# Kernel tuning notes

Hardware: AMD Instinct MI355X
Metric: run time of the kernel (lower is better)

## Reference

```python
import jax, jax.numpy as jnp
import numpy as np

N_NODES = 50000
N_EDGES = 800000
MUL = 32            # multiplicity of 0e and 1o feature irreps
N_SPECIES = 4       # node_attr = 4x0e one-hot
N_BASIS = 8         # radial basis scalars
N_HID = 8           # invariant_neurons
AVG_NEIGH = 16.0
INV_SQRT3 = 1.0 / np.sqrt(3.0).astype(np.float32)


def setup_inputs() -> dict:
    key = jax.random.key(0)
    ks = jax.random.split(key, 16)
    x = jax.random.normal(ks[0], (N_NODES, MUL * 4), jnp.float32)  # 32x0e + 32x1o
    species = jax.random.randint(ks[1], (N_NODES,), 0, N_SPECIES)
    node_attr = jax.nn.one_hot(species, N_SPECIES, dtype=jnp.float32)
    edge_embedding = jax.random.normal(ks[2], (N_EDGES, N_BASIS), jnp.float32)
    edge_attr = jax.random.normal(ks[3], (N_EDGES, 4), jnp.float32)  # 1x0e + 1x1o
    edge_index = jax.random.randint(ks[4], (2, N_EDGES), 0, N_NODES)
    # learned params
    W_lin1_s = jax.random.normal(ks[5], (MUL, MUL), jnp.float32)
    W_lin1_v = jax.random.normal(ks[6], (MUL, MUL), jnp.float32)
    fc_w1 = jax.random.normal(ks[7], (N_BASIS, N_HID), jnp.float32)
    fc_w2 = jax.random.normal(ks[8], (N_HID, 4 * MUL), jnp.float32)  # tp.weight_numel = 4*MUL
    W_lin2_s = jax.random.normal(ks[9], (2 * MUL, MUL), jnp.float32)  # mid simplify: 64x0e
    W_lin2_v = jax.random.normal(ks[10], (2 * MUL, MUL), jnp.float32)  # 64x1o
    W_sc_s = jax.random.normal(ks[11], (MUL, N_SPECIES, MUL), jnp.float32)
    W_sc_v = jax.random.normal(ks[12], (MUL, N_SPECIES, MUL), jnp.float32)
    return dict(node_features=x, node_attr=node_attr, edge_embedding=edge_embedding,
                edge_attr=edge_attr, edge_index=edge_index,
                W_lin1_s=W_lin1_s, W_lin1_v=W_lin1_v, fc_w1=fc_w1, fc_w2=fc_w2,
                W_lin2_s=W_lin2_s, W_lin2_v=W_lin2_v, W_sc_s=W_sc_s, W_sc_v=W_sc_v)


def _forward(node_features, node_attr, edge_embedding, edge_attr, edge_index,
             W_lin1_s, W_lin1_v, fc_w1, fc_w2, W_lin2_s, W_lin2_v, W_sc_s, W_sc_v):
    n = node_features.shape[0]
    xs = node_features[:, :MUL]                       # [N, 32] scalars (0e)
    xv = node_features[:, MUL:].reshape(n, MUL, 3)    # [N, 32, 3] vectors (1o)

    # self-connection: FullyConnectedTensorProduct(feat, 4x0e -> feat), uvw weights
    sc_norm = 1.0 / np.sqrt(MUL * N_SPECIES).astype(np.float32)
    sc_s = jnp.einsum('nu,nv,uvw->nw', xs, node_attr, W_sc_s) * sc_norm
    sc_v = jnp.einsum('nui,nv,uvw->nwi', xv, node_attr, W_sc_v) * sc_norm

    # linear_1: per-irrep channel mixing, 1/sqrt(fan_in)
    l1n = 1.0 / np.sqrt(MUL).astype(np.float32)
    ys = (xs @ W_lin1_s) * l1n
    yv = jnp.einsum('nui,uw->nwi', xv, W_lin1_v) * l1n

    # radial MLP -> per-edge tensor-product weights (4 paths x MUL)
    h = jax.nn.silu((edge_embedding @ fc_w1) / np.sqrt(N_BASIS).astype(np.float32))
    w = (h @ fc_w2) / np.sqrt(N_HID).astype(np.float32)  # [E, 128]
    w00, w01, w10, w11 = jnp.split(w, 4, axis=1)          # instruction order (0,0),(0,1),(1,0),(1,1)

    src = edge_index[0]
    dst = edge_index[1]
    es = ys[src]                                          # [E, 32]
    ev = yv[src]                                          # [E, 32, 3]
    a0 = edge_attr[:, 0]                                  # [E]    0e
    a1 = edge_attr[:, 1:4]                                # [E, 3] 1o

    # per-edge weighted uvu tensor product paths
    o_s_a = w00 * es * a0[:, None]                                       # 0e x 0e -> 0e
    o_s_b = w11 * jnp.einsum('eui,ei->eu', ev, a1) * INV_SQRT3           # 1o x 1o -> 0e
    o_v_a = (w01 * es)[:, :, None] * a1[:, None, :]                      # 0e x 1o -> 1o
    o_v_b = w10[:, :, None] * ev * a0[:, None, None]                     # 1o x 0e -> 1o

    # scatter-sum to destination nodes
    mid_s = jax.ops.segment_sum(jnp.concatenate([o_s_a, o_s_b], axis=1), dst, num_segments=n)
    mid_v = jax.ops.segment_sum(jnp.concatenate([o_v_a, o_v_b], axis=1), dst, num_segments=n)
    inv = 1.0 / np.sqrt(AVG_NEIGH).astype(np.float32)
    mid_s = mid_s * inv   # [N, 64]
    mid_v = mid_v * inv   # [N, 64, 3]

    # linear_2: 64x0e+64x1o -> 32x0e+32x1o
    l2n = 1.0 / np.sqrt(2 * MUL).astype(np.float32)
    out_s = (mid_s @ W_lin2_s) * l2n + sc_s
    out_v = jnp.einsum('nui,uw->nwi', mid_v, W_lin2_v) * l2n + sc_v
    return jnp.concatenate([out_s, out_v.reshape(n, MUL * 3)], axis=1)


def reference(node_features, node_attr, edge_embedding, edge_attr, edge_index,
              W_lin1_s, W_lin1_v, fc_w1, fc_w2, W_lin2_s, W_lin2_v, W_sc_s, W_sc_v):
    return _forward(node_features, node_attr, edge_embedding, edge_attr, edge_index,
                    W_lin1_s, W_lin1_v, fc_w1, fc_w2, W_lin2_s, W_lin2_v, W_sc_s, W_sc_v)
```

## Files before the change

### kernel.cpp

```cpp
#include <hip/hip_runtime.h>
#include <hip/hip_bf16.h>

#define N_NODES 50000
#define N_EDGES 800000
#define CAP 64
#define NODE_BLOCKS 1250
#define BUCKET_BLOCKS (N_EDGES/256)

__device__ __forceinline__ unsigned short f2bf(float f) {
    union { float f; unsigned u; } t; t.f = f;
    unsigned r = t.u + 0x7FFF + ((t.u >> 16) & 1);
    return (unsigned short)(r >> 16);
}

__global__ __launch_bounds__(256) void bucket_kernel(
    const int* __restrict__ eidx,
    int* __restrict__ counts, int* __restrict__ bucket)
{
    const int e = blockIdx.x * 256 + threadIdx.x;
    const int dst = eidx[N_EDGES + e];
    const int slot = atomicAdd(&counts[dst], 1);
    if (slot < CAP) bucket[(long)dst * CAP + slot] = e;
}

__global__ __launch_bounds__(256) void node_kernel(
    const float* __restrict__ x, const float* __restrict__ attr,
    const float* __restrict__ W1s, const float* __restrict__ W1v,
    const float* __restrict__ Wscs, const float* __restrict__ Wscv,
    unsigned short* __restrict__ ysvh, float* __restrict__ out)
{
    __shared__ float shm[10240];
    const int tid = threadIdx.x;
    const int nl = tid >> 5;
    const int w  = tid & 31;

    float w1s[32], w1v[32];
    #pragma unroll
    for (int u = 0; u < 32; ++u) {
        w1s[u] = W1s[u*32 + w];
        w1v[u] = W1v[u*32 + w];
    }
    #pragma unroll
    for (int i = 0; i < 4; ++i) {
        ((float4*)(shm + 2048))[tid + i*256] = ((const float4*)Wscs)[tid + i*256];
        ((float4*)(shm + 6144))[tid + i*256] = ((const float4*)Wscv)[tid + i*256];
    }

    const float l1n = 0.17677669529663687f;
    const float scn = 0.08838834764831843f;

    for (int batch = 0; batch < 5; ++batch) {
        const int node0 = blockIdx.x * 40 + batch * 8;
        float* xbuf = shm + (batch & 1) * 1024;
        ((float4*)xbuf)[tid] = ((const float4*)(x + (long)node0 * 128))[tid];
        __syncthreads();

        const int node = node0 + nl;
        const float* at = attr + (long)node * 4;
        int sp = 0;
        if (at[1] > 0.5f) sp = 1;
        if (at[2] > 0.5f) sp = 2;
        if (at[3] > 0.5f) sp = 3;

        const float* lx   = xbuf + nl * 128;
        const float* lscs = shm + 2048 + sp * 32;
        const float* lscv = shm + 6144 + sp * 32;

        float ys = 0.f, yv0 = 0.f, yv1 = 0.f, yv2 = 0.f;
        float ss = 0.f, sv0 = 0.f, sv1 = 0.f, sv2 = 0.f;
        #pragma unroll
        for (int u4 = 0; u4 < 8; ++u4) {
            const float4 xs4 = ((const float4*)lx)[u4];
            const float4 q0  = ((const float4*)(lx + 32))[u4*3 + 0];
            const float4 q1  = ((const float4*)(lx + 32))[u4*3 + 1];
            const float4 q2  = ((const float4*)(lx + 32))[u4*3 + 2];
            const float xsv[4]  = {xs4.x, xs4.y, xs4.z, xs4.w};
            const float xvv[12] = {q0.x,q0.y,q0.z,q0.w,
                                   q1.x,q1.y,q1.z,q1.w,
                                   q2.x,q2.y,q2.z,q2.w};
            #pragma unroll
            for (int j = 0; j < 4; ++j) {
                const int u = u4*4 + j;
                const float wss = lscs[u*128 + w];
                const float wsv = lscv[u*128 + w];
                ys  += xsv[j] * w1s[u];
                yv0 += xvv[3*j+0] * w1v[u];
                yv1 += xvv[3*j+1] * w1v[u];
                yv2 += xvv[3*j+2] * w1v[u];
                ss  += xsv[j] * wss;
                sv0 += xvv[3*j+0] * wsv;
                sv1 += xvv[3*j+1] * wsv;
                sv2 += xvv[3*j+2] * wsv;
            }
        }

        uint2 pk;
        pk.x = (unsigned)f2bf(ys  * l1n) | ((unsigned)f2bf(yv0 * l1n) << 16);
        pk.y = (unsigned)f2bf(yv1 * l1n) | ((unsigned)f2bf(yv2 * l1n) << 16);
        *(uint2*)(ysvh + (long)node * 128 + w * 4) = pk;

        float* op = out + (long)node * 128;
        op[w] = ss * scn;
        op[32 + 3*w + 0] = sv0 * scn;
        op[32 + 3*w + 1] = sv1 * scn;
        op[32 + 3*w + 2] = sv2 * scn;
    }
}

__global__ __launch_bounds__(256) void agg_kernel(
    const float* __restrict__ ee, const float* __restrict__ eattr,
    const int* __restrict__ eidx,
    const float* __restrict__ fcw1, const float* __restrict__ fcw2,
    const float* __restrict__ W2s, const float* __restrict__ W2v,
    const unsigned short* __restrict__ ysvh,
    const int* __restrict__ counts, const int* __restrict__ bucket,
    float* __restrict__ out)
{
    __shared__ float hrec[8][32 * 12];
    __shared__ float mid[8][256];

    const int tid = threadIdx.x;
    const int nl = tid >> 5;
    const int u  = tid & 31;
    const int node = blockIdx.x * 8 + nl;
    const float inv_sqrt8 = 0.35355339059327373f;

    float f2r[8][4];
    #pragma unroll
    for (int j = 0; j < 8; ++j) {
        f2r[j][0] = fcw2[j*128 + u];
        f2r[j][1] = fcw2[j*128 + 32 + u];
        f2r[j][2] = fcw2[j*128 + 64 + u];
        f2r[j][3] = fcw2[j*128 + 96 + u];
    }

    const int cnt = min(counts[node], CAP);
    int e0 = bucket[(long)node * CAP + u];
    const bool dummy = (u >= cnt);
    if (dummy) e0 = 0;
    int s0 = eidx[e0];

    {
        const float4 ea = ((const float4*)(ee + (long)e0 * 8))[0];
        const float4 eb = ((const float4*)(ee + (long)e0 * 8))[1];
        const float4 at = ((const float4*)eattr)[e0];
        const float eev[8] = {ea.x, ea.y, ea.z, ea.w, eb.x, eb.y, eb.z, eb.w};
        float* hr = hrec[nl] + u * 12;
        float h[8];
        #pragma unroll
        for (int j = 0; j < 8; ++j) {
            float pre = 0.f;
            #pragma unroll
            for (int b = 0; b < 8; ++b) pre += eev[b] * fcw1[b*8 + j];
            pre *= inv_sqrt8;
            const float s = pre / (1.f + __expf(-pre)) * inv_sqrt8;
            h[j] = dummy ? 0.f : s;
        }
        ((float4*)hr)[0] = make_float4(h[0], h[1], h[2], h[3]);
        ((float4*)hr)[1] = make_float4(h[4], h[5], h[6], h[7]);
        ((float4*)hr)[2] = at;
    }

    float msa = 0.f, msb = 0.f;
    float va0 = 0.f, va1 = 0.f, va2 = 0.f;
    float vb0 = 0.f, vb1 = 0.f, vb2 = 0.f;

    #define ACCUM(HA, HB, AT, Y)                                             \
    {                                                                        \
        const float es = __uint_as_float((Y).x << 16);                       \
        const float ex = __uint_as_float((Y).x & 0xffff0000u);               \
        const float ey = __uint_as_float((Y).y << 16);                       \
        const float ez = __uint_as_float((Y).y & 0xffff0000u);               \
        const float hh[8] = {HA.x,HA.y,HA.z,HA.w,HB.x,HB.y,HB.z,HB.w};       \
        float w00=0.f, w01=0.f, w10=0.f, w11=0.f;                            \
        _Pragma("unroll")                                                    \
        for (int j = 0; j < 8; ++j) {                                        \
            w00 += hh[j]*f2r[j][0]; w01 += hh[j]*f2r[j][1];                  \
            w10 += hh[j]*f2r[j][2]; w11 += hh[j]*f2r[j][3];                  \
        }                                                                    \
        const float a0 = AT.x, a1x = AT.y, a1y = AT.z, a1z = AT.w;           \
        msa += w00 * es * a0;                                                \
        msb += w11 * (ex*a1x + ey*a1y + ez*a1z);                             \
        const float t = w01 * es;                                            \
        va0 += t*a1x; va1 += t*a1y; va2 += t*a1z;                            \
        const float s = w10 * a0;                                            \
        vb0 += s*ex; vb1 += s*ey; vb2 += s*ez;                               \
    }

    #define GATHER(SLOT) \
        (*(const uint2*)(ysvh + (long)__shfl(s0, (SLOT), 32) * 128 + u * 4))

    const int c0 = min(cnt, 32);
    {
        uint2 y0 = GATHER(0), y1 = GATHER(1), y2 = GATHER(2), y3 = GATHER(3);
        for (int k = 0; k < c0; k += 4) {
            const int kn = (k + 4) & 31;
            const uint2 n0 = GATHER(kn);
            const uint2 n1 = GATHER(kn + 1);
            const uint2 n2 = GATHER(kn + 2);
            const uint2 n3 = GATHER(kn + 3);
            const float4* h0p = (const float4*)(hrec[nl] + (k + 0) * 12);
            const float4* h1p = (const float4*)(hrec[nl] + (k + 1) * 12);
            const float4* h2p = (const float4*)(hrec[nl] + (k + 2) * 12);
            const float4* h3p = (const float4*)(hrec[nl] + (k + 3) * 12);
            const float4 A0 = h0p[0], B0 = h0p[1], T0 = h0p[2];
            const float4 A1 = h1p[0], B1 = h1p[1], T1 = h1p[2];
            const float4 A2 = h2p[0], B2 = h2p[1], T2 = h2p[2];
            const float4 A3 = h3p[0], B3 = h3p[1], T3 = h3p[2];
            ACCUM(A0, B0, T0, y0)
            ACCUM(A1, B1, T1, y1)
            ACCUM(A2, B2, T2, y2)
            ACCUM(A3, B3, T3, y3)
            y0 = n0; y1 = n1; y2 = n2; y3 = n3;
        }
    }

    if (cnt > 32) {
        int be = bucket[(long)node * CAP + 32 + u];
        if (32 + u >= cnt) be = 0;
        for (int k = 32; k < cnt; ++k) {
            const int e = __shfl(be, k - 32, 32);
            const int s = eidx[e];
            const float4 ea = ((const float4*)(ee + (long)e * 8))[0];
            const float4 eb = ((const float4*)(ee + (long)e * 8))[1];
            const float4 at = ((const float4*)eattr)[e];
            const float eev[8] = {ea.x, ea.y, ea.z, ea.w, eb.x, eb.y, eb.z, eb.w};
            float h[8];
            #pragma unroll
            for (int j = 0; j < 8; ++j) {
                float pre = 0.f;
                #pragma unroll
                for (int b = 0; b < 8; ++b) pre += eev[b] * fcw1[b*8 + j];
                pre *= inv_sqrt8;
                h[j] = pre / (1.f + __expf(-pre)) * inv_sqrt8;
            }
            const float4 HA = make_float4(h[0], h[1], h[2], h[3]);
            const float4 HB = make_float4(h[4], h[5], h[6], h[7]);
            const uint2 y = *(const uint2*)(ysvh + (long)s * 128 + u * 4);
            ACCUM(HA, HB, at, y)
        }
    }
    #undef GATHER
    #undef ACCUM

    msb *= 0.5773502691896258f;

    float* m = mid[nl];
    m[u]       = msa;
    m[32 + u]  = msb;
    m[64  + u*3 + 0] = va0;  m[64  + u*3 + 1] = va1;  m[64  + u*3 + 2] = va2;
    m[160 + u*3 + 0] = vb0;  m[160 + u*3 + 1] = vb1;  m[160 + u*3 + 2] = vb2;

    float os = 0.f, ov0 = 0.f, ov1 = 0.f, ov2 = 0.f;
    #pragma unroll 8
    for (int q = 0; q < 32; ++q) {
        const float wsa = W2s[q*32 + u];
        const float wsb = W2s[(32 + q)*32 + u];
        os += m[q] * wsa + m[32 + q] * wsb;
        const float wva = W2v[q*32 + u];
        const float wvb = W2v[(32 + q)*32 + u];
        ov0 += m[64 + q*3 + 0] * wva + m[160 + q*3 + 0] * wvb;
        ov1 += m[64 + q*3 + 1] * wva + m[160 + q*3 + 1] * wvb;
        ov2 += m[64 + q*3 + 2] * wva + m[160 + q*3 + 2] * wvb;
    }

    const float sc = 0.03125f;
    float* op = out + (long)node * 128;
    op[u]            += os  * sc;
    op[32 + 3*u + 0] += ov0 * sc;
    op[32 + 3*u + 1] += ov1 * sc;
    op[32 + 3*u + 2] += ov2 * sc;
}

extern "C" void kernel_launch(void* const* d_in, const int* in_sizes, int n_in,
                              void* d_out, int out_size, void* d_ws, size_t ws_size,
                              hipStream_t stream) {
    const float* x     = (const float*)d_in[0];
    const float* attr  = (const float*)d_in[1];
    const float* ee    = (const float*)d_in[2];
    const float* eattr = (const float*)d_in[3];
    const int*   eidx  = (const int*)  d_in[4];
    const float* W1s   = (const float*)d_in[5];
    const float* W1v   = (const float*)d_in[6];
    const float* fcw1  = (const float*)d_in[7];
    const float* fcw2  = (const float*)d_in[8];
    const float* W2s   = (const float*)d_in[9];
    const float* W2v   = (const float*)d_in[10];
    const float* Wscs  = (const float*)d_in[11];
    const float* Wscv  = (const float*)d_in[12];

    float* out = (float*)d_out;

    unsigned short* ysvh = (unsigned short*)d_ws;
    int*   counts = (int*)(ysvh + (long)N_NODES * 128);
    int*   bucket = counts + N_NODES;

    hipMemsetAsync(counts, 0, N_NODES * sizeof(int), stream);
    bucket_kernel<<<BUCKET_BLOCKS, 256, 0, stream>>>(eidx, counts, bucket);
    node_kernel<<<NODE_BLOCKS, 256, 0, stream>>>(x, attr, W1s, W1v, Wscs, Wscv,
                                                 ysvh, out);
    agg_kernel<<<N_NODES/8, 256, 0, stream>>>(ee, eattr, eidx, fcw1, fcw2,
                                              W2s, W2v, ysvh, counts, bucket, out);
}
```

Baseline: 319.7 us.

## Fuse edge bucketing into node kernel and pad per-node counters

Merges the edge-bucketing pass and the node linear pass into one launch, with separate block ranges, so the two independent stages can overlap and one launch is saved. Each bucketing thread now handles two edges. Counters are padded to a 16-int stride so atomics on different nodes land on separate cache lines. The self-connection weights are read straight from global memory instead of being staged in shared memory, which shrinks LDS use. Bucket capacity drops from 64 to 48 to save memory, so correctness now relies on no node having more than 48 incoming edges. The padded counters also enlarge the memset.

```diff
diff --git a/kernel.cpp b/kernel.cpp
--- a/kernel.cpp
+++ b/kernel.cpp
@@ -3,9 +3,10 @@
 
 #define N_NODES 50000
 #define N_EDGES 800000
-#define CAP 64
+#define CAP 48
+#define CSTRIDE 16
 #define NODE_BLOCKS 1250
-#define BUCKET_BLOCKS (N_EDGES/256)
+#define BUCKET_BLOCKS 1563
 
 __device__ __forceinline__ unsigned short f2bf(float f) {
     union { float f; unsigned u; } t; t.f = f;
@@ -13,97 +14,97 @@
     return (unsigned short)(r >> 16);
 }
 
-__global__ __launch_bounds__(256) void bucket_kernel(
-    const int* __restrict__ eidx,
-    int* __restrict__ counts, int* __restrict__ bucket)
-{
-    const int e = blockIdx.x * 256 + threadIdx.x;
-    const int dst = eidx[N_EDGES + e];
-    const int slot = atomicAdd(&counts[dst], 1);
-    if (slot < CAP) bucket[(long)dst * CAP + slot] = e;
-}
-
-__global__ __launch_bounds__(256) void node_kernel(
+__global__ __launch_bounds__(256) void prep_kernel(
     const float* __restrict__ x, const float* __restrict__ attr,
     const float* __restrict__ W1s, const float* __restrict__ W1v,
     const float* __restrict__ Wscs, const float* __restrict__ Wscv,
+    const int* __restrict__ eidx,
+    int* __restrict__ counts, int* __restrict__ bucket,
     unsigned short* __restrict__ ysvh, float* __restrict__ out)
 {
-    __shared__ float shm[10240];
+    __shared__ float shm[2048];
     const int tid = threadIdx.x;
-    const int nl = tid >> 5;
-    const int w  = tid & 31;
-
-    float w1s[32], w1v[32];
-    #pragma unroll
-    for (int u = 0; u < 32; ++u) {
-        w1s[u] = W1s[u*32 + w];
-        w1v[u] = W1v[u*32 + w];
-    }
-    #pragma unroll
-    for (int i = 0; i < 4; ++i) {
-        ((float4*)(shm + 2048))[tid + i*256] = ((const float4*)Wscs)[tid + i*256];
-        ((float4*)(shm + 6144))[tid + i*256] = ((const float4*)Wscv)[tid + i*256];
-    }
-
-    const float l1n = 0.17677669529663687f;
-    const float scn = 0.08838834764831843f;
-
-    for (int batch = 0; batch < 5; ++batch) {
-        const int node0 = blockIdx.x * 40 + batch * 8;
-        float* xbuf = shm + (batch & 1) * 1024;
-        ((float4*)xbuf)[tid] = ((const float4*)(x + (long)node0 * 128))[tid];
-        __syncthreads();
-
-        const int node = node0 + nl;
-        const float* at = attr + (long)node * 4;
-        int sp = 0;
-        if (at[1] > 0.5f) sp = 1;
-        if (at[2] > 0.5f) sp = 2;
-        if (at[3] > 0.5f) sp = 3;
-
-        const float* lx   = xbuf + nl * 128;
-        const float* lscs = shm + 2048 + sp * 32;
-        const float* lscv = shm + 6144 + sp * 32;
-
-        float ys = 0.f, yv0 = 0.f, yv1 = 0.f, yv2 = 0.f;
-        float ss = 0.f, sv0 = 0.f, sv1 = 0.f, sv2 = 0.f;
+
+    if (blockIdx.x < NODE_BLOCKS) {
+        const int nl = tid >> 5;
+        const int w  = tid & 31;
+
+        float w1s[32], w1v[32];
         #pragma unroll
-        for (int u4 = 0; u4 < 8; ++u4) {
-            const float4 xs4 = ((const float4*)lx)[u4];
-            const float4 q0  = ((const float4*)(lx + 32))[u4*3 + 0];
-            const float4 q1  = ((const float4*)(lx + 32))[u4*3 + 1];
-            const float4 q2  = ((const float4*)(lx + 32))[u4*3 + 2];
-            const float xsv[4]  = {xs4.x, xs4.y, xs4.z, xs4.w};
-            const float xvv[12] = {q0.x,q0.y,q0.z,q0.w,
-                                   q1.x,q1.y,q1.z,q1.w,
-                                   q2.x,q2.y,q2.z,q2.w};
+        for (int u = 0; u < 32; ++u) {
+            w1s[u] = W1s[u*32 + w];
+            w1v[u] = W1v[u*32 + w];
+        }
+
+        const float l1n = 0.17677669529663687f;
+        const float scn = 0.08838834764831843f;
+
+        for (int batch = 0; batch < 5; ++batch) {
+            const int node0 = blockIdx.x * 40 + batch * 8;
+            float* xbuf = shm + (batch & 1) * 1024;
+            ((float4*)xbuf)[tid] = ((const float4*)(x + (long)node0 * 128))[tid];
+            __syncthreads();
+
+            const int node = node0 + nl;
+            const float* at = attr + (long)node * 4;
+            int sp = 0;
+            if (at[1] > 0.5f) sp = 1;
+            if (at[2] > 0.5f) sp = 2;
+            if (at[3] > 0.5f) sp = 3;
+
+            const float* lx   = xbuf + nl * 128;
+            const float* gscs = Wscs + sp * 32 + w;
+            const float* gscv = Wscv + sp * 32 + w;
+
+            float ys = 0.f, yv0 = 0.f, yv1 = 0.f, yv2 = 0.f;
+            float ss = 0.f, sv0 = 0.f, sv1 = 0.f, sv2 = 0.f;
             #pragma unroll
-            for (int j = 0; j < 4; ++j) {
-                const int u = u4*4 + j;
-                const float wss = lscs[u*128 + w];
-                const float wsv = lscv[u*128 + w];
-                ys  += xsv[j] * w1s[u];
-                yv0 += xvv[3*j+0] * w1v[u];
-                yv1 += xvv[3*j+1] * w1v[u];
-                yv2 += xvv[3*j+2] * w1v[u];
-                ss  += xsv[j] * wss;
-                sv0 += xvv[3*j+0] * wsv;
-                sv1 += xvv[3*j+1] * wsv;
-                sv2 += xvv[3*j+2] * wsv;
+            for (int u4 = 0; u4 < 8; ++u4) {
+                const float4 xs4 = ((const float4*)lx)[u4];
+                const float4 q0  = ((const float4*)(lx + 32))[u4*3 + 0];
+                const float4 q1  = ((const float4*)(lx + 32))[u4*3 + 1];
+                const float4 q2  = ((const float4*)(lx + 32))[u4*3 + 2];
+                const float xsv[4]  = {xs4.x, xs4.y, xs4.z, xs4.w};
+                const float xvv[12] = {q0.x,q0.y,q0.z,q0.w,
+                                       q1.x,q1.y,q1.z,q1.w,
+                                       q2.x,q2.y,q2.z,q2.w};
+                #pragma unroll
+                for (int j = 0; j < 4; ++j) {
+                    const int u = u4*4 + j;
+                    const float wss = gscs[u*128];
+                    const float wsv = gscv[u*128];
+                    ys  += xsv[j] * w1s[u];
+                    yv0 += xvv[3*j+0] * w1v[u];
+                    yv1 += xvv[3*j+1] * w1v[u];
+                    yv2 += xvv[3*j+2] * w1v[u];
+                    ss  += xsv[j] * wss;
+                    sv0 += xvv[3*j+0] * wsv;
+                    sv1 += xvv[3*j+1] * wsv;
+                    sv2 += xvv[3*j+2] * wsv;
+                }
             }
-        }
-
-        uint2 pk;
-        pk.x = (unsigned)f2bf(ys  * l1n) | ((unsigned)f2bf(yv0 * l1n) << 16);
-        pk.y = (unsigned)f2bf(yv1 * l1n) | ((unsigned)f2bf(yv2 * l1n) << 16);
-        *(uint2*)(ysvh + (long)node * 128 + w * 4) = pk;
-
-        float* op = out + (long)node * 128;
-        op[w] = ss * scn;
-        op[32 + 3*w + 0] = sv0 * scn;
-        op[32 + 3*w + 1] = sv1 * scn;
-        op[32 + 3*w + 2] = sv2 * scn;
+
+            uint2 pk;
+            pk.x = (unsigned)f2bf(ys  * l1n) | ((unsigned)f2bf(yv0 * l1n) << 16);
+            pk.y = (unsigned)f2bf(yv1 * l1n) | ((unsigned)f2bf(yv2 * l1n) << 16);
+            *(uint2*)(ysvh + (long)node * 128 + w * 4) = pk;
+
+            float* op = out + (long)node * 128;
+            op[w] = ss * scn;
+            op[32 + 3*w + 0] = sv0 * scn;
+            op[32 + 3*w + 1] = sv1 * scn;
+            op[32 + 3*w + 2] = sv2 * scn;
+        }
+    } else {
+        const int gid = (blockIdx.x - NODE_BLOCKS) * 256 + tid;
+        if (gid < N_EDGES/2) {
+            const int d0 = eidx[N_EDGES + gid];
+            const int d1 = eidx[N_EDGES + gid + N_EDGES/2];
+            const int s0 = atomicAdd(&counts[d0 * CSTRIDE], 1);
+            const int s1 = atomicAdd(&counts[d1 * CSTRIDE], 1);
+            if (s0 < CAP) bucket[(long)d0 * CAP + s0] = gid;
+            if (s1 < CAP) bucket[(long)d1 * CAP + s1] = gid + N_EDGES/2;
+        }
     }
 }
 
@@ -134,11 +135,11 @@
         f2r[j][3] = fcw2[j*128 + 96 + u];
     }
 
-    const int cnt = min(counts[node], CAP);
-    int e0 = bucket[(long)node * CAP + u];
+    const int cnt = min(counts[node * CSTRIDE], CAP);
+    int e0 = bucket[(long)node * CAP + min(u, CAP-1)];
     const bool dummy = (u >= cnt);
     if (dummy) e0 = 0;
-    int s0 = eidx[e0];
+    const int s0 = dummy ? 0 : eidx[e0];
 
     {
         const float4 ea = ((const float4*)(ee + (long)e0 * 8))[0];
@@ -216,7 +217,7 @@
     }
 
     if (cnt > 32) {
-        int be = bucket[(long)node * CAP + 32 + u];
+        int be = bucket[(long)node * CAP + min(32 + u, CAP-1)];
         if (32 + u >= cnt) be = 0;
         for (int k = 32; k < cnt; ++k) {
             const int e = __shfl(be, k - 32, 32);
@@ -293,12 +294,11 @@
 
     unsigned short* ysvh = (unsigned short*)d_ws;
     int*   counts = (int*)(ysvh + (long)N_NODES * 128);
-    int*   bucket = counts + N_NODES;
-
-    hipMemsetAsync(counts, 0, N_NODES * sizeof(int), stream);
-    bucket_kernel<<<BUCKET_BLOCKS, 256, 0, stream>>>(eidx, counts, bucket);
-    node_kernel<<<NODE_BLOCKS, 256, 0, stream>>>(x, attr, W1s, W1v, Wscs, Wscv,
-                                                 ysvh, out);
+    int*   bucket = counts + (long)N_NODES * CSTRIDE;
+
+    hipMemsetAsync(counts, 0, (long)N_NODES * CSTRIDE * sizeof(int), stream);
+    prep_kernel<<<NODE_BLOCKS + BUCKET_BLOCKS, 256, 0, stream>>>(
+        x, attr, W1s, W1v, Wscs, Wscv, eidx, counts, bucket, ysvh, out);
     agg_kernel<<<N_NODES/8, 256, 0, stream>>>(ee, eattr, eidx, fcw1, fcw2,
                                               W2s, W2v, ysvh, counts, bucket, out);
 }
```

Result: faster. 289.7 us (-9.4%).
